# Kernel optimization log

Measured on AMD Instinct MI355X. Metric: run time of the kernel, lower is better.

## Reference

```python
import jax, jax.numpy as jnp
import numpy as np

B, T, HID = 8, 1024, 2048
H, D = 16, 128          # num_attention_heads, head_dim (num_kv_heads = 1)
Q_RANK, KV_RANK = 128, 64
EPS = 1e-6
MIN_VAL = -1e9          # fp32 branch of create_causal_padding_mask


def _rmsnorm(x, w, eps=EPS):
    return x * jax.lax.rsqrt(jnp.mean(x * x, axis=-1, keepdims=True) + eps) * w


def _rope(x, cos, sin):
    x1, x2 = jnp.split(x, 2, axis=-1)
    return jnp.concatenate([x1 * cos - x2 * sin, x2 * cos + x1 * sin], axis=-1)


def setup_inputs() -> dict:
    key = jax.random.key(0)
    ks = jax.random.split(key, 12)
    s = lambda fan_in: 1.0 / np.sqrt(fan_in)
    return {
        'hidden_states': jax.random.normal(ks[0], (B, T, HID), jnp.float32),
        'cos_g': jax.random.uniform(ks[1], (1, T, 1, D // 2), jnp.float32, -1.0, 1.0),
        'sin_g': jax.random.uniform(ks[2], (1, T, 1, D // 2), jnp.float32, -1.0, 1.0),
        'cos_l': jax.random.uniform(ks[3], (1, T, 1, D // 2), jnp.float32, -1.0, 1.0),
        'sin_l': jax.random.uniform(ks[4], (1, T, 1, D // 2), jnp.float32, -1.0, 1.0),
        'Wq_a': jax.random.normal(ks[5], (HID, Q_RANK), jnp.float32) * s(HID),
        'bq_a': jnp.zeros((Q_RANK,), jnp.float32),
        'Wq_b': jax.random.normal(ks[6], (Q_RANK, H * D), jnp.float32) * s(Q_RANK),
        'bq_b': jnp.zeros((H * D,), jnp.float32),
        'Wkv_a': jax.random.normal(ks[7], (HID, KV_RANK), jnp.float32) * s(HID),
        'bkv_a': jnp.zeros((KV_RANK,), jnp.float32),
        'Wkv_b': jax.random.normal(ks[8], (KV_RANK, 2 * D), jnp.float32) * s(KV_RANK),
        'bkv_b': jnp.zeros((2 * D,), jnp.float32),
        'q_norm_w': jnp.ones((D,), jnp.float32),
        'kv_norm_w': jnp.ones((KV_RANK,), jnp.float32),
        'Wo': jax.random.normal(ks[9], (H * D, HID), jnp.float32) * s(H * D),
        'nope_logit': jnp.array([-2.0], jnp.float32),
        'gl_logit': jnp.array([np.log(0.01 / 0.99)], jnp.float32),
        'attention_mask': jnp.ones((B, T), jnp.int32),
    }


def reference(hidden_states, cos_g, sin_g, cos_l, sin_l,
              Wq_a, bq_a, Wq_b, bq_b, Wkv_a, bkv_a, Wkv_b, bkv_b,
              q_norm_w, kv_norm_w, Wo, nope_logit, gl_logit, attention_mask):
    h = hidden_states
    # learned global/local RoPE blend
    a = jax.nn.sigmoid(gl_logit).reshape(1, 1, 1, 1)
    cos = cos_g * a + cos_l * (1.0 - a)
    sin = sin_g * a + sin_l * (1.0 - a)

    # LoRA q path: q_b(RMSNorm(q_a(h)))
    q = _rmsnorm(h @ Wq_a + bq_a, q_norm_w) @ Wq_b + bq_b      # [B,T,H*D]
    q = q.reshape(B, T, H, D)
    q_pe = _rope(q, cos, sin)

    # LoRA kv path: kv_b(RMSNorm(kv_a(h)))  (single kv head)
    kv = _rmsnorm(h @ Wkv_a + bkv_a, kv_norm_w) @ Wkv_b + bkv_b  # [B,T,2*D]
    k, v = jnp.split(kv, 2, axis=-1)                            # [B,T,D] each
    k_pe = _rope(k.reshape(B, T, 1, D), cos, sin)[:, :, 0, :]   # [B,T,D]

    # nope/rope alpha mix
    na = jax.nn.sigmoid(nope_logit).reshape(1, 1, 1, 1)
    q_f = na * q + (1.0 - na) * q_pe                            # [B,T,H,D]
    k_f = na[..., 0] * k + (1.0 - na[..., 0]) * k_pe            # [B,T,D]

    # causal + padding additive mask
    causal = jnp.triu(jnp.ones((T, T), bool), k=1)              # [T,T]
    pad = (attention_mask == 0)[:, None, None, :]               # [B,1,1,T]
    add_mask = jnp.where(causal[None, None] | pad, MIN_VAL, 0.0).astype(h.dtype)

    scale = D ** -0.5
    scores = jnp.einsum('bthd,bsd->bhts', q_f, k_f) * scale + add_mask
    attn = jax.nn.softmax(scores, axis=-1)                      # [B,H,T,T]
    out = jnp.einsum('bhts,bsd->bthd', attn, v)                 # [B,T,H,D]
    return out.reshape(B, T, H * D) @ Wo
```

## Files before the change

kernel.cpp:

```cpp
#include <hip/hip_runtime.h>
#include <hip/hip_bf16.h>

typedef __attribute__((ext_vector_type(8))) short bf16x8;
typedef __attribute__((ext_vector_type(4))) float f32x4;
typedef __attribute__((ext_vector_type(4))) unsigned short us4;

#define DEV __device__ __forceinline__

constexpr int Bc = 8, Tc = 1024, HIDc = 2048, Hc = 16, Dc = 128;
constexpr int ROWSc = Bc * Tc;

DEV unsigned short f2bfb(float x) {
  union { float f; unsigned u; } v; v.f = x;
  unsigned r = v.u + 0x7fffu + ((v.u >> 16) & 1u);
  return (unsigned short)(r >> 16);
}
DEV float bfb2f(unsigned short b) {
  union { unsigned u; float f; } v; v.u = ((unsigned)b) << 16; return v.f;
}
DEV float fexp2(float x) { return __builtin_amdgcn_exp2f(x); }
DEV unsigned pkbf(float lo, float hi) {
  union { float f; unsigned u; } a, b; a.f = lo; b.f = hi;
  return ((b.u + 0x8000u) & 0xffff0000u) | ((a.u + 0x8000u) >> 16);
}

DEV void gload16(const void* g, void* l) {
  __builtin_amdgcn_global_load_lds(
      (const __attribute__((address_space(1))) unsigned int*)g,
      (__attribute__((address_space(3))) unsigned int*)l, 16, 0, 0);
}


__global__ void k_blend(const float* __restrict__ cg, const float* __restrict__ sg,
                        const float* __restrict__ cl, const float* __restrict__ sl,
                        const float* __restrict__ gl,
                        float* __restrict__ cosb, float* __restrict__ sinb) {
  int u = blockIdx.x * 256 + threadIdx.x;
  if (u >= Tc * 64) return;
  float a = 1.0f / (1.0f + __expf(-gl[0]));
  cosb[u] = cg[u] * a + cl[u] * (1.0f - a);
  sinb[u] = sg[u] * a + sl[u] * (1.0f - a);
}

__global__ void k_zero(unsigned short* __restrict__ p, int n) {
  int i = blockIdx.x * 256 + threadIdx.x;
  if (i < n) p[i] = 0;
}

__global__ __launch_bounds__(256) void k_transpose(const float* __restrict__ in,
                                                   unsigned short* __restrict__ out,
                                                   int R, int C) {
  __shared__ float tile[32][33];
  int tx = threadIdx.x & 31, ty = threadIdx.x >> 5;
  int r0 = blockIdx.y * 32, c0 = blockIdx.x * 32;
#pragma unroll
  for (int i = 0; i < 4; i++)
    tile[ty + i * 8][tx] = in[(size_t)(r0 + ty + i * 8) * C + c0 + tx];
  __syncthreads();
#pragma unroll
  for (int i = 0; i < 4; i++) {
    int rr = ty + i * 8;
    out[(size_t)(c0 + rr) * R + r0 + tx] = f2bfb(tile[tx][rr]);
  }
}


__global__ __launch_bounds__(256) void k_gemm1(const float* __restrict__ A,
                                               const unsigned short* __restrict__ Bt,
                                               float* __restrict__ C0,
                                               float* __restrict__ C1) {
  constexpr int K = 2048, N = 256, KH = 1024, NT = KH / 32;
  __shared__ __align__(16) unsigned short Als[2][64 * 32];
  __shared__ __align__(16) unsigned short Bls[2][128 * 32];
  int lin = blockIdx.x;
  int wg = (lin & 7) * 64 + (lin >> 3);
  int ksl = wg & 1;
  int nti = (wg >> 1) & 1;
  int mti = wg >> 2;
  int m0 = mti * 64, n0 = nti * 128, k0 = ksl * KH;
  float* C = ksl ? C1 : C0;
  int tid = threadIdx.x, lane = tid & 63, wc = tid >> 6;
  int ar = tid >> 2, akc = (tid & 3) * 8;
  const float* Ag = A + (size_t)(m0 + ar) * K + k0 + akc;
  const unsigned short* Bg0 = Bt + (size_t)(n0 + ar) * K + k0 + akc;
  const unsigned short* Bg1 = Bt + (size_t)(n0 + 64 + ar) * K + k0 + akc;
  f32x4 acc[4][2];
  f32x4 zz = {0.f, 0.f, 0.f, 0.f};
#pragma unroll
  for (int m = 0; m < 4; m++)
#pragma unroll
    for (int n = 0; n < 2; n++) acc[m][n] = zz;
  int fr = lane & 15, fk = (lane >> 4) * 8;

  float4 a0 = *(const float4*)(Ag);
  float4 a1 = *(const float4*)(Ag + 4);
  gload16(Bg0, &Bls[0][tid * 8]);
  gload16(Bg1, &Bls[0][2048 + tid * 8]);
  {
    us4 c0v = { f2bfb(a0.x), f2bfb(a0.y), f2bfb(a0.z), f2bfb(a0.w) };
    us4 c1v = { f2bfb(a1.x), f2bfb(a1.y), f2bfb(a1.z), f2bfb(a1.w) };
    *(us4*)&Als[0][ar * 32 + akc] = c0v;
    *(us4*)&Als[0][ar * 32 + akc + 4] = c1v;
  }
  a0 = *(const float4*)(Ag + 32);
  a1 = *(const float4*)(Ag + 36);
  __syncthreads();

  for (int t = 0; t < NT; t++) {
    int cur = t & 1, nxt = cur ^ 1;
    if (t + 1 < NT) {
      gload16(Bg0 + (t + 1) * 32, &Bls[nxt][tid * 8]);
      gload16(Bg1 + (t + 1) * 32, &Bls[nxt][2048 + tid * 8]);
    }
    bf16x8 af[4], bfv[2];
#pragma unroll
    for (int i = 0; i < 4; i++)
      af[i] = *(const bf16x8*)&Als[cur][(i * 16 + fr) * 32 + fk];
#pragma unroll
    for (int i = 0; i < 2; i++)
      bfv[i] = *(const bf16x8*)&Bls[cur][(wc * 32 + i * 16 + fr) * 32 + fk];
    __builtin_amdgcn_s_setprio(1);
#pragma unroll
    for (int m = 0; m < 4; m++)
#pragma unroll
      for (int n = 0; n < 2; n++)
        acc[m][n] = __builtin_amdgcn_mfma_f32_16x16x32_bf16(af[m], bfv[n], acc[m][n], 0, 0, 0);
    __builtin_amdgcn_s_setprio(0);
    if (t + 1 < NT) {
      us4 d0 = { f2bfb(a0.x), f2bfb(a0.y), f2bfb(a0.z), f2bfb(a0.w) };
      us4 d1 = { f2bfb(a1.x), f2bfb(a1.y), f2bfb(a1.z), f2bfb(a1.w) };
      *(us4*)&Als[nxt][ar * 32 + akc] = d0;
      *(us4*)&Als[nxt][ar * 32 + akc + 4] = d1;
    }
    if (t + 2 < NT) {
      a0 = *(const float4*)(Ag + (t + 2) * 32);
      a1 = *(const float4*)(Ag + (t + 2) * 32 + 4);
    }
    __syncthreads();
  }
  int gg = lane >> 4;
#pragma unroll
  for (int m = 0; m < 4; m++)
#pragma unroll
    for (int n = 0; n < 2; n++)
#pragma unroll
      for (int r = 0; r < 4; r++) {
        size_t row = (size_t)m0 + m * 16 + gg * 4 + r;
        size_t col = (size_t)n0 + wc * 32 + n * 16 + fr;
        C[row * N + col] = acc[m][n][r];
      }
}


__global__ __launch_bounds__(512, 2) void k_gemm3(const unsigned short* __restrict__ A,
                                                  const unsigned short* __restrict__ Bt,
                                                  float* __restrict__ C) {
  constexpr int K = 2048, N = 2048, NT = K / 64;
  __shared__ __align__(16) unsigned short Als[2][2][8192];
  __shared__ __align__(16) unsigned short Bls[2][2][8192];
  int lin = blockIdx.x;
  int wg = (lin & 7) * 32 + (lin >> 3);
  int m0 = (wg >> 3) * 256, n0 = (wg & 7) * 256;
  int tid = threadIdx.x, lane = tid & 63, wave = tid >> 6;
  int wm = wave >> 2, wn = wave & 3;
  int g = lane >> 4, c = lane & 15;

  int rb = tid >> 2;
  int sch = (tid & 3) ^ ((tid >> 3) & 3);
  const unsigned short* Ag = A + (size_t)(m0 + rb) * K + sch * 8;
  const unsigned short* Bg = Bt + (size_t)(n0 + rb) * K + sch * 8;
  const int gsw = (g ^ ((c >> 1) & 3)) * 8;

  f32x4 acc[8][4];
  f32x4 zz = {0.f, 0.f, 0.f, 0.f};
#pragma unroll
  for (int mi = 0; mi < 8; mi++)
#pragma unroll
    for (int ni = 0; ni < 4; ni++) acc[mi][ni] = zz;

#pragma unroll
  for (int sl = 0; sl < 2; sl++) {
    gload16(Ag + sl * 32, &Als[0][sl][tid * 8]);
    gload16(Ag + (size_t)128 * K + sl * 32, &Als[0][sl][4096 + tid * 8]);
    gload16(Bg + sl * 32, &Bls[0][sl][tid * 8]);
    gload16(Bg + (size_t)128 * K + sl * 32, &Bls[0][sl][4096 + tid * 8]);
  }

  for (int t = 0; t < NT; ++t) {
    int buf = t & 1, nb = buf ^ 1;
    bool nl = (t + 1 < NT);
    int nkt = (t + 1) * 64;
#pragma unroll
    for (int sl = 0; sl < 2; sl++) {
      if (sl == 0 || nl) {
        asm volatile("s_waitcnt vmcnt(4)" ::: "memory");
      } else {
        asm volatile("s_waitcnt vmcnt(0)" ::: "memory");
      }
      __builtin_amdgcn_sched_barrier(0);
      __builtin_amdgcn_s_barrier();
      __builtin_amdgcn_sched_barrier(0);
      const unsigned short* As_ = &Als[buf][sl][0];
      const unsigned short* Bs_ = &Bls[buf][sl][0];
      bf16x8 af[8], bfv[4];
#pragma unroll
      for (int mi = 0; mi < 8; mi++)
        af[mi] = *(const bf16x8*)&As_[(wm * 128 + mi * 16 + c) * 32 + gsw];
#pragma unroll
      for (int ni = 0; ni < 4; ni++)
        bfv[ni] = *(const bf16x8*)&Bs_[(wn * 64 + ni * 16 + c) * 32 + gsw];
      if (nl) {
        gload16(Ag + nkt + sl * 32, &Als[nb][sl][tid * 8]);
        gload16(Ag + (size_t)128 * K + nkt + sl * 32, &Als[nb][sl][4096 + tid * 8]);
      }
      __builtin_amdgcn_s_setprio(1);
#pragma unroll
      for (int mi = 0; mi < 8; mi++) {
        acc[mi][0] = __builtin_amdgcn_mfma_f32_16x16x32_bf16(af[mi], bfv[0], acc[mi][0], 0, 0, 0);
        acc[mi][1] = __builtin_amdgcn_mfma_f32_16x16x32_bf16(af[mi], bfv[1], acc[mi][1], 0, 0, 0);
      }
      __builtin_amdgcn_s_setprio(0);
      if (nl) {
        gload16(Bg + nkt + sl * 32, &Bls[nb][sl][tid * 8]);
        gload16(Bg + (size_t)128 * K + nkt + sl * 32, &Bls[nb][sl][4096 + tid * 8]);
      }
      __builtin_amdgcn_s_setprio(1);
#pragma unroll
      for (int mi = 0; mi < 8; mi++) {
        acc[mi][2] = __builtin_amdgcn_mfma_f32_16x16x32_bf16(af[mi], bfv[2], acc[mi][2], 0, 0, 0);
        acc[mi][3] = __builtin_amdgcn_mfma_f32_16x16x32_bf16(af[mi], bfv[3], acc[mi][3], 0, 0, 0);
      }
      __builtin_amdgcn_s_setprio(0);
    }
  }

#pragma unroll
  for (int mi = 0; mi < 8; mi++)
#pragma unroll
    for (int ni = 0; ni < 4; ni++)
#pragma unroll
      for (int r = 0; r < 4; r++) {
        size_t row = (size_t)m0 + wm * 128 + mi * 16 + g * 4 + r;
        size_t col = (size_t)n0 + wn * 64 + ni * 16 + c;
        C[row * N + col] = acc[mi][ni][r];
      }
}


__global__ __launch_bounds__(256) void k_gemm2q(const unsigned short* __restrict__ A,
                                                const unsigned short* __restrict__ Bt,
                                                const float* __restrict__ bqb,
                                                const float* __restrict__ cosb,
                                                const float* __restrict__ sinb,
                                                const float* __restrict__ nl,
                                                unsigned short* __restrict__ Qf) {
  constexpr int K = 128, N = 2048, NT = 4;
  __shared__ __align__(16) unsigned short As[2][4096];
  __shared__ __align__(16) unsigned short Bs[2][4096];
  __shared__ __align__(16) unsigned short Qt[128 * 128];
  int lin = blockIdx.x;
  int wg = (lin & 7) * 128 + (lin >> 3);
  int m0 = (wg >> 4) * 128, n0 = (wg & 15) * 128;
  int h = n0 >> 7;
  int b = m0 >> 10, t0 = m0 & 1023;
  int tid = threadIdx.x;
  int lane = tid & 63;
  int wave = tid >> 6;
  int wr = wave >> 1, wc = wave & 1;
  int srow = tid >> 2;
  int skc = (tid & 3) * 8;
  const unsigned short* Ag0 = A + (size_t)(m0 + srow) * K + skc;
  const unsigned short* Ag1 = A + (size_t)(m0 + 64 + srow) * K + skc;
  const unsigned short* Bg0 = Bt + (size_t)(n0 + srow) * K + skc;
  const unsigned short* Bg1 = Bt + (size_t)(n0 + 64 + srow) * K + skc;
  f32x4 acc[4][4];
  f32x4 zz = {0.f, 0.f, 0.f, 0.f};
#pragma unroll
  for (int m = 0; m < 4; m++)
#pragma unroll
    for (int n = 0; n < 4; n++) acc[m][n] = zz;
  int fr = lane & 15, fk = (lane >> 4) * 8;

  gload16(Ag0, &As[0][tid * 8]);
  gload16(Ag1, &As[0][2048 + tid * 8]);
  gload16(Bg0, &Bs[0][tid * 8]);
  gload16(Bg1, &Bs[0][2048 + tid * 8]);
  __syncthreads();

  for (int t = 0; t < NT; t++) {
    int cur = t & 1, nxt = cur ^ 1;
    if (t + 1 < NT) {
      int kt = (t + 1) * 32;
      gload16(Ag0 + kt, &As[nxt][tid * 8]);
      gload16(Ag1 + kt, &As[nxt][2048 + tid * 8]);
      gload16(Bg0 + kt, &Bs[nxt][tid * 8]);
      gload16(Bg1 + kt, &Bs[nxt][2048 + tid * 8]);
    }
    bf16x8 af[4], bfv[4];
#pragma unroll
    for (int i = 0; i < 4; i++)
      af[i] = *(const bf16x8*)&As[cur][(wr * 64 + i * 16 + fr) * 32 + fk];
#pragma unroll
    for (int i = 0; i < 4; i++)
      bfv[i] = *(const bf16x8*)&Bs[cur][(wc * 64 + i * 16 + fr) * 32 + fk];
    __builtin_amdgcn_s_setprio(1);
#pragma unroll
    for (int m = 0; m < 4; m++)
#pragma unroll
      for (int n = 0; n < 4; n++)
        acc[m][n] = __builtin_amdgcn_mfma_f32_16x16x32_bf16(af[m], bfv[n], acc[m][n], 0, 0, 0);
    __builtin_amdgcn_s_setprio(0);
    __syncthreads();
  }
  int gg = lane >> 4;
#pragma unroll
  for (int n = 0; n < 4; n++) {
    int col = wc * 64 + n * 16 + fr;
    float bias = bqb[h * 128 + col];
    int ch = col >> 3, wi = col & 7;
#pragma unroll
    for (int m = 0; m < 4; m++)
#pragma unroll
      for (int r = 0; r < 4; r++) {
        int lrow = wr * 64 + m * 16 + gg * 4 + r;
        Qt[lrow * 128 + ((ch ^ (lrow & 7)) << 3) + wi] = f2bfb(acc[m][n][r] + bias);
      }
  }
  __syncthreads();
  const float SCLQ = 0.08838834764831845f * 1.4426950408889634f;
  float na = 1.0f / (1.0f + __expf(-nl[0]));
  float nb = 1.0f - na;
#pragma unroll
  for (int it = 0; it < 4; it++) {
    int task = it * 256 + tid;
    int lrow = task >> 3, cp = task & 7;
    int t = t0 + lrow;
    bf16x8 v1 = *(const bf16x8*)&Qt[lrow * 128 + ((cp ^ (lrow & 7)) << 3)];
    bf16x8 v2 = *(const bf16x8*)&Qt[lrow * 128 + (((cp + 8) ^ (lrow & 7)) << 3)];
    float4 cA = *(const float4*)(cosb + t * 64 + cp * 8);
    float4 cB = *(const float4*)(cosb + t * 64 + cp * 8 + 4);
    float4 sA = *(const float4*)(sinb + t * 64 + cp * 8);
    float4 sB = *(const float4*)(sinb + t * 64 + cp * 8 + 4);
    float cv[8] = {cA.x, cA.y, cA.z, cA.w, cB.x, cB.y, cB.z, cB.w};
    float sv[8] = {sA.x, sA.y, sA.z, sA.w, sB.x, sB.y, sB.z, sB.w};
    float f1[8], f2[8];
#pragma unroll
    for (int j = 0; j < 8; j++) {
      float q1 = bfb2f((unsigned short)v1[j]);
      float q2 = bfb2f((unsigned short)v2[j]);
      float p1 = q1 * cv[j] - q2 * sv[j];
      float p2 = q2 * cv[j] + q1 * sv[j];
      f1[j] = (na * q1 + nb * p1) * SCLQ;
      f2[j] = (na * q2 + nb * p2) * SCLQ;
    }
    unsigned short* ob = Qf + ((size_t)(b * Hc + h) * Tc + t) * Dc + cp * 8;
    us4 o0 = {f2bfb(f1[0]), f2bfb(f1[1]), f2bfb(f1[2]), f2bfb(f1[3])};
    us4 o1 = {f2bfb(f1[4]), f2bfb(f1[5]), f2bfb(f1[6]), f2bfb(f1[7])};
    us4 o2 = {f2bfb(f2[0]), f2bfb(f2[1]), f2bfb(f2[2]), f2bfb(f2[3])};
    us4 o3 = {f2bfb(f2[4]), f2bfb(f2[5]), f2bfb(f2[6]), f2bfb(f2[7])};
    *(us4*)(ob) = o0;
    *(us4*)(ob + 4) = o1;
    *(us4*)(ob + 64) = o2;
    *(us4*)(ob + 68) = o3;
  }
}


__global__ __launch_bounds__(256) void k_gemm2kv(const unsigned short* __restrict__ A,
                                                 const unsigned short* __restrict__ Bt,
                                                 const float* __restrict__ bkvb,
                                                 const float* __restrict__ cosb,
                                                 const float* __restrict__ sinb,
                                                 const float* __restrict__ nl,
                                                 unsigned short* __restrict__ Kf,
                                                 unsigned short* __restrict__ Vt) {
  __shared__ __align__(16) unsigned short As2[64 * 64];
  __shared__ __align__(16) unsigned short Bs2[256 * 64];
  __shared__ __align__(16) unsigned short KVt[64 * 256];
  int m0 = blockIdx.x * 64;
  int b = m0 >> 10, t0 = m0 & 1023;
  int tid = threadIdx.x, lane = tid & 63, wc = tid >> 6;
  int fr = lane & 15, gg = lane >> 4;
#pragma unroll
  for (int p = 0; p < 2; p++) {
    int slot = p * 256 + tid;
    int row = slot >> 3, chpos = slot & 7;
    gload16(A + (size_t)(m0 + row) * 64 + ((chpos ^ (row & 7)) << 3),
            &As2[slot * 8]);
  }
#pragma unroll
  for (int p = 0; p < 8; p++) {
    int slot = p * 256 + tid;
    int row = slot >> 3, chpos = slot & 7;
    gload16(Bt + (size_t)row * 64 + ((chpos ^ (row & 7)) << 3),
            &Bs2[slot * 8]);
  }
  __syncthreads();
  f32x4 acc[4][4];
  f32x4 zz = {0.f, 0.f, 0.f, 0.f};
#pragma unroll
  for (int m = 0; m < 4; m++)
#pragma unroll
    for (int n = 0; n < 4; n++) acc[m][n] = zz;
#pragma unroll
  for (int ks = 0; ks < 2; ks++) {
    bf16x8 af[4], bfv[4];
#pragma unroll
    for (int m = 0; m < 4; m++) {
      int row = m * 16 + fr;
      af[m] = *(const bf16x8*)&As2[row * 64 + (((ks * 4 + gg) ^ (row & 7)) << 3)];
    }
#pragma unroll
    for (int n = 0; n < 4; n++) {
      int row = wc * 64 + n * 16 + fr;
      bfv[n] = *(const bf16x8*)&Bs2[row * 64 + (((ks * 4 + gg) ^ (row & 7)) << 3)];
    }
#pragma unroll
    for (int m = 0; m < 4; m++)
#pragma unroll
      for (int n = 0; n < 4; n++)
        acc[m][n] = __builtin_amdgcn_mfma_f32_16x16x32_bf16(af[m], bfv[n], acc[m][n], 0, 0, 0);
  }
#pragma unroll
  for (int n = 0; n < 4; n++) {
    int col = wc * 64 + n * 16 + fr;
    float bias = bkvb[col];
#pragma unroll
    for (int m = 0; m < 4; m++)
#pragma unroll
      for (int r = 0; r < 4; r++) {
        int lrow = m * 16 + gg * 4 + r;
        KVt[lrow * 256 + col] = f2bfb(acc[m][n][r] + bias);
      }
  }
  __syncthreads();
  float na = 1.0f / (1.0f + __expf(-nl[0]));
  float nb = 1.0f - na;
#pragma unroll
  for (int it = 0; it < 16; it++) {
    int idx = it * 256 + tid;
    int row = idx >> 6, d = idx & 63;
    int t = t0 + row;
    float k1 = bfb2f(KVt[row * 256 + d]);
    float k2 = bfb2f(KVt[row * 256 + 64 + d]);
    float cv = cosb[t * 64 + d], sv = sinb[t * 64 + d];
    float p1 = k1 * cv - k2 * sv;
    float p2 = k2 * cv + k1 * sv;
    unsigned short* kb = Kf + ((size_t)(b * Tc) + t) * Dc;
    kb[d] = f2bfb(na * k1 + nb * p1);
    kb[64 + d] = f2bfb(na * k2 + nb * p2);
  }
  {
    int d = tid & 127, half = tid >> 7;
    unsigned short* vb = Vt + ((size_t)(b * Dc) + d) * Tc + t0 + half * 32;
#pragma unroll
    for (int j = 0; j < 8; j++) {
      int tl = half * 32 + j * 4;
      us4 o = { KVt[(tl + 0) * 256 + 128 + d], KVt[(tl + 1) * 256 + 128 + d],
                KVt[(tl + 2) * 256 + 128 + d], KVt[(tl + 3) * 256 + 128 + d] };
      *(us4*)(vb + j * 4) = o;
    }
  }
}


__global__ __launch_bounds__(256) void k_norm(const float* __restrict__ A1,
                                              const float* __restrict__ A1b,
                                              const float* __restrict__ bqa,
                                              const float* __restrict__ bkva,
                                              const float* __restrict__ qw,
                                              const float* __restrict__ kvw,
                                              unsigned short* __restrict__ Qn,
                                              unsigned short* __restrict__ Kvn) {
  int wave = threadIdx.x >> 6, lane = threadIdx.x & 63;
  int row = blockIdx.x * 4 + wave;
  const float* a = A1 + (size_t)row * 256;
  const float* a2 = A1b + (size_t)row * 256;
  float x0 = a[lane] + a2[lane] + bqa[lane];
  float x1 = a[64 + lane] + a2[64 + lane] + bqa[64 + lane];
  float ss = x0 * x0 + x1 * x1;
#pragma unroll
  for (int off = 1; off < 64; off <<= 1) ss += __shfl_xor(ss, off);
  float sc = rsqrtf(ss * (1.0f / 128.0f) + 1e-6f);
  Qn[(size_t)row * 128 + lane] = f2bfb(x0 * sc * qw[lane]);
  Qn[(size_t)row * 128 + 64 + lane] = f2bfb(x1 * sc * qw[64 + lane]);
  float y = a[128 + lane] + a2[128 + lane] + bkva[lane];
  float s2 = y * y;
#pragma unroll
  for (int off = 1; off < 64; off <<= 1) s2 += __shfl_xor(s2, off);
  float sc2 = rsqrtf(s2 * (1.0f / 64.0f) + 1e-6f);
  Kvn[(size_t)row * 64 + lane] = f2bfb(y * sc2 * kvw[lane]);
}


__global__ __launch_bounds__(512, 1) void k_attn(const unsigned short* __restrict__ Qf,
                                                 const unsigned short* __restrict__ Kf,
                                                 const unsigned short* __restrict__ Vt,
                                                 const int* __restrict__ amask,
                                                 unsigned short* __restrict__ O) {
  __shared__ __align__(16) unsigned short Ks[2][64 * 128];
  __shared__ __align__(16) unsigned short Vs[2][128 * 64];
  __shared__ __align__(16) unsigned short Plds[8][32 * 64];
  __shared__ int s_anyzero;

  int bid = blockIdx.x;
  int b = bid & 7;
  int pr = (bid >> 3) & 1;
  int h = bid >> 4;
  int tid = threadIdx.x;
  int wave = tid >> 6, lane = tid & 63;
  int g = lane >> 4, c = lane & 15;

  const unsigned short* Kp = Kf + (size_t)b * Tc * Dc;
  const unsigned short* Vp = Vt + (size_t)b * Dc * Tc;
  const int* mp = amask + b * Tc;
  char* PwB = (char*)&Plds[wave][0];
  f32x4 zz = {0.f, 0.f, 0.f, 0.f};

  if (tid == 0) s_anyzero = 0;
  __syncthreads();
  if (mp[tid] == 0 || mp[tid + 512] == 0) s_anyzero = 1;
  __syncthreads();
  bool anyz = (s_anyzero != 0);

  int kr_ = tid >> 3, kc_ = tid & 7;
  int vr_ = tid >> 2, vc_ = tid & 3;
  int kidx0 = kr_ * 128 + ((kc_ ^ (kr_ & 7)) << 3);
  int kidx1 = kr_ * 128 + (((kc_ + 8) ^ (kr_ & 7)) << 3);
  int vidx0 = vr_ * 64 + ((vc_ ^ (vr_ & 7)) << 3);
  int vidx1 = vr_ * 64 + (((vc_ + 4) ^ (vr_ & 7)) << 3);

  int c7s = (c & 7) << 4;
  int g4 = g * 4;

  for (int pass = 0; pass < 2; pass++) {
    int sp = (pass == 0) ? pr : 3 - pr;
    int qw0 = sp * 256 + wave * 32;
    int nt = (sp + 1) * 4;
    const unsigned short* Qp = Qf + ((size_t)(b * Hc + h) * Tc + qw0) * Dc;
    bf16x8 qfr[2][4];
#pragma unroll
    for (int m = 0; m < 2; m++)
#pragma unroll
      for (int ks = 0; ks < 4; ks++)
        qfr[m][ks] = *(const bf16x8*)(Qp + (size_t)(m * 16 + c) * Dc + ks * 32 + g * 8);

    f32x4 Oacc[2][8];
#pragma unroll
    for (int m = 0; m < 2; m++)
#pragma unroll
      for (int i = 0; i < 8; i++) Oacc[m][i] = zz;
    float m_r[2] = {-1e30f, -1e30f};
    float l_r[2] = {0.f, 0.f};

    bf16x8 krg[2], vrg[2];
    krg[0] = *(const bf16x8*)(Kp + (size_t)kr_ * Dc + kc_ * 8);
    krg[1] = *(const bf16x8*)(Kp + (size_t)kr_ * Dc + kc_ * 8 + 64);
    vrg[0] = *(const bf16x8*)(Vp + (size_t)vr_ * Tc + vc_ * 8);
    vrg[1] = *(const bf16x8*)(Vp + (size_t)vr_ * Tc + vc_ * 8 + 32);
    __syncthreads();
    *(bf16x8*)&Ks[0][kidx0] = krg[0];
    *(bf16x8*)&Ks[0][kidx1] = krg[1];
    *(bf16x8*)&Vs[0][vidx0] = vrg[0];
    *(bf16x8*)&Vs[0][vidx1] = vrg[1];
    __syncthreads();

    for (int st = 0; st < nt; st++) {
      int cur = st & 1;
      int s0 = st << 6;
      if (st + 1 < nt) {
        int s1 = s0 + 64;
        krg[0] = *(const bf16x8*)(Kp + (size_t)(s1 + kr_) * Dc + kc_ * 8);
        krg[1] = *(const bf16x8*)(Kp + (size_t)(s1 + kr_) * Dc + kc_ * 8 + 64);
        vrg[0] = *(const bf16x8*)(Vp + (size_t)vr_ * Tc + s1 + vc_ * 8);
        vrg[1] = *(const bf16x8*)(Vp + (size_t)vr_ * Tc + s1 + vc_ * 8 + 32);
      }

      if (s0 <= qw0 + 31) {
        const unsigned short* Kc = &Ks[cur][0];
        const unsigned short* Vc = &Vs[cur][0];

        f32x4 S[2][4];
#pragma unroll
        for (int m = 0; m < 2; m++)
#pragma unroll
          for (int j = 0; j < 4; j++) S[m][j] = zz;
        __builtin_amdgcn_s_setprio(1);
#pragma unroll
        for (int ks = 0; ks < 4; ks++)
#pragma unroll
          for (int j = 0; j < 4; j++) {
            bf16x8 kfr = *(const bf16x8*)&Kc[(j * 16 + c) * 128 + (((ks * 4 + g) ^ (c & 7)) << 3)];
            S[0][j] = __builtin_amdgcn_mfma_f32_16x16x32_bf16(kfr, qfr[0][ks], S[0][j], 0, 0, 0);
            S[1][j] = __builtin_amdgcn_mfma_f32_16x16x32_bf16(kfr, qfr[1][ks], S[1][j], 0, 0, 0);
          }
        __builtin_amdgcn_s_setprio(0);

        if (anyz) {
#pragma unroll
          for (int j = 0; j < 4; j++)
#pragma unroll
            for (int r = 0; r < 4; r++) {
              float madd = (mp[s0 + j * 16 + g4 + r] == 0) ? -2e9f : 0.0f;
              S[0][j][r] += madd;
              S[1][j][r] += madd;
            }
        }
        if (s0 + 63 > qw0) {
#pragma unroll
          for (int j = 0; j < 4; j++) {
            int kk = s0 + j * 16 + g4;
#pragma unroll
            for (int r = 0; r < 4; r++) {
#pragma unroll
              for (int m = 0; m < 2; m++)
                if (kk + r > qw0 + m * 16 + c) S[m][j][r] = -1e30f;
            }
          }
        }

        float tmax[2];
#pragma unroll
        for (int m = 0; m < 2; m++) {
          float t0 = fmaxf(fmaxf(S[m][0][0], S[m][0][1]), fmaxf(S[m][0][2], S[m][0][3]));
          float t1 = fmaxf(fmaxf(S[m][1][0], S[m][1][1]), fmaxf(S[m][1][2], S[m][1][3]));
          float t2 = fmaxf(fmaxf(S[m][2][0], S[m][2][1]), fmaxf(S[m][2][2], S[m][2][3]));
          float t3 = fmaxf(fmaxf(S[m][3][0], S[m][3][1]), fmaxf(S[m][3][2], S[m][3][3]));
          float t = fmaxf(fmaxf(t0, t1), fmaxf(t2, t3));
          t = fmaxf(t, __shfl_xor(t, 16));
          t = fmaxf(t, __shfl_xor(t, 32));
          tmax[m] = t;
        }
        bool upd = (tmax[0] > m_r[0] + 11.0f) || (tmax[1] > m_r[1] + 11.0f);
        if (__any(upd)) {
#pragma unroll
          for (int m = 0; m < 2; m++) {
            float mn = fmaxf(m_r[m], tmax[m]);
            float al = fexp2(m_r[m] - mn);
            m_r[m] = mn;
            l_r[m] *= al;
#pragma unroll
            for (int r = 0; r < 4; r++) {
              float alr = __shfl(al, (lane & 48) | (g4 + r));
#pragma unroll
              for (int j2 = 0; j2 < 8; j2++) Oacc[m][j2][r] *= alr;
            }
          }
        }

#pragma unroll
        for (int m = 0; m < 2; m++) {
          int rowb = (m * 16 + c) * 128;
#pragma unroll
          for (int j = 0; j < 4; j++) {
            float e0 = fexp2(S[m][j][0] - m_r[m]);
            float e1 = fexp2(S[m][j][1] - m_r[m]);
            float e2 = fexp2(S[m][j][2] - m_r[m]);
            float e3 = fexp2(S[m][j][3] - m_r[m]);
            l_r[m] += (e0 + e1) + (e2 + e3);
            uint2 w;
            w.x = pkbf(e0, e1);
            w.y = pkbf(e2, e3);
            int inrow = (j * 32 + g * 8) ^ c7s;
            *(uint2*)(PwB + rowb + inrow) = w;
          }
        }

        asm volatile("s_waitcnt lgkmcnt(0)" ::: "memory");
        bf16x8 pa[2][2];
#pragma unroll
        for (int m = 0; m < 2; m++)
#pragma unroll
          for (int sk = 0; sk < 2; sk++)
            pa[m][sk] = *(const bf16x8*)(PwB + (m * 16 + c) * 128 + (((sk * 64 + g * 16)) ^ c7s));
        __builtin_amdgcn_s_setprio(1);
#pragma unroll
        for (int sk = 0; sk < 2; sk++)
#pragma unroll
          for (int j2 = 0; j2 < 8; j2++) {
            int row = j2 * 16 + c;
            bf16x8 vfr = *(const bf16x8*)&Vc[row * 64 + (((sk * 4 + g) ^ (row & 7)) << 3)];
            Oacc[0][j2] = __builtin_amdgcn_mfma_f32_16x16x32_bf16(pa[0][sk], vfr, Oacc[0][j2], 0, 0, 0);
            Oacc[1][j2] = __builtin_amdgcn_mfma_f32_16x16x32_bf16(pa[1][sk], vfr, Oacc[1][j2], 0, 0, 0);
          }
        __builtin_amdgcn_s_setprio(0);
      }

      if (st + 1 < nt) {
        int nxt = cur ^ 1;
        *(bf16x8*)&Ks[nxt][kidx0] = krg[0];
        *(bf16x8*)&Ks[nxt][kidx1] = krg[1];
        *(bf16x8*)&Vs[nxt][vidx0] = vrg[0];
        *(bf16x8*)&Vs[nxt][vidx1] = vrg[1];
      }
      __syncthreads();
    }

#pragma unroll
    for (int m = 0; m < 2; m++) {
      float lt = l_r[m];
      lt += __shfl_xor(lt, 16);
      lt += __shfl_xor(lt, 32);
      float inv = 1.0f / lt;
#pragma unroll
      for (int r = 0; r < 4; r++) {
        float invr = __shfl(inv, (lane & 48) | (g4 + r));
        int qr = qw0 + m * 16 + g4 + r;
        unsigned short* ob = O + ((size_t)(b * Tc) + qr) * HIDc + h * Dc;
#pragma unroll
        for (int j2 = 0; j2 < 8; j2++) ob[j2 * 16 + c] = f2bfb(Oacc[m][j2][r] * invr);
      }
    }
  }
}


extern "C" void kernel_launch(void* const* d_in, const int* in_sizes, int n_in,
                              void* d_out, int out_size, void* d_ws, size_t ws_size,
                              hipStream_t stream) {
  const float* h = (const float*)d_in[0];
  const float* cg = (const float*)d_in[1];
  const float* sg = (const float*)d_in[2];
  const float* cl = (const float*)d_in[3];
  const float* sl = (const float*)d_in[4];
  const float* Wq_a = (const float*)d_in[5];
  const float* bq_a = (const float*)d_in[6];
  const float* Wq_b = (const float*)d_in[7];
  const float* bq_b = (const float*)d_in[8];
  const float* Wkv_a = (const float*)d_in[9];
  const float* bkv_a = (const float*)d_in[10];
  const float* Wkv_b = (const float*)d_in[11];
  const float* bkv_b = (const float*)d_in[12];
  const float* qw = (const float*)d_in[13];
  const float* kvw = (const float*)d_in[14];
  const float* Wo = (const float*)d_in[15];
  const float* nl = (const float*)d_in[16];
  const float* gl = (const float*)d_in[17];
  const int* am = (const int*)d_in[18];
  float* out = (float*)d_out;
  char* ws = (char*)d_ws;

  const size_t o_hB = 0;
  const size_t o_A1b = 33554432;
  const size_t o_Qf = 67108864;
  const size_t o_A1 = 100663296;
  const size_t o_Qn = 109051904;
  const size_t o_Kvn = 111149056;
  const size_t o_Kf = 116391936;
  const size_t o_Vt = 118489088;
  const size_t o_W1t = 120586240;
  const size_t o_Wqbt = 121634816;
  const size_t o_Wkbt = 122159104;
  const size_t o_Wot = 122191872;
  const size_t o_cos = 130580480;
  const size_t o_sin = 130842624;

  unsigned short* Obuf = (unsigned short*)(ws + o_hB);
  float* A1b = (float*)(ws + o_A1b);
  unsigned short* Qf = (unsigned short*)(ws + o_Qf);
  float* A1 = (float*)(ws + o_A1);
  unsigned short* Qn = (unsigned short*)(ws + o_Qn);
  unsigned short* Kvn = (unsigned short*)(ws + o_Kvn);
  unsigned short* Kf = (unsigned short*)(ws + o_Kf);
  unsigned short* Vt = (unsigned short*)(ws + o_Vt);
  unsigned short* W1t = (unsigned short*)(ws + o_W1t);
  unsigned short* Wqbt = (unsigned short*)(ws + o_Wqbt);
  unsigned short* Wkbt = (unsigned short*)(ws + o_Wkbt);
  unsigned short* Wot = (unsigned short*)(ws + o_Wot);
  float* cosb = (float*)(ws + o_cos);
  float* sinb = (float*)(ws + o_sin);

  (void)in_sizes; (void)n_in; (void)out_size; (void)ws_size;

  k_blend<<<256, 256, 0, stream>>>(cg, sg, cl, sl, gl, cosb, sinb);
  k_zero<<<512, 256, 0, stream>>>(W1t + (size_t)192 * 2048, 64 * 2048);
  k_transpose<<<dim3(4, 64), 256, 0, stream>>>(Wq_a, W1t, 2048, 128);
  k_transpose<<<dim3(2, 64), 256, 0, stream>>>(Wkv_a, W1t + (size_t)128 * 2048, 2048, 64);
  k_transpose<<<dim3(64, 4), 256, 0, stream>>>(Wq_b, Wqbt, 128, 2048);
  k_transpose<<<dim3(8, 2), 256, 0, stream>>>(Wkv_b, Wkbt, 64, 256);
  k_transpose<<<dim3(64, 64), 256, 0, stream>>>(Wo, Wot, 2048, 2048);

  k_gemm1<<<512, 256, 0, stream>>>(h, W1t, A1, A1b);
  k_norm<<<2048, 256, 0, stream>>>(A1, A1b, bq_a, bkv_a, qw, kvw, Qn, Kvn);
  k_gemm2q<<<1024, 256, 0, stream>>>(Qn, Wqbt, bq_b, cosb, sinb, nl, Qf);
  k_gemm2kv<<<128, 256, 0, stream>>>(Kvn, Wkbt, bkv_b, cosb, sinb, nl, Kf, Vt);
  k_attn<<<256, 512, 0, stream>>>(Qf, Kf, Vt, am, Obuf);
  k_gemm3<<<256, 512, 0, stream>>>(Obuf, Wot, out);
}
```

Measured before the change: 206.2 us.

## Deepen output GEMM pipeline to four-stage ring of 32-wide K slices

The Wo projection GEMM moves from a double buffer of 64-wide K tiles (two 32-wide sub-slices each) to a four-slot ring of 32-wide K slices. Global loads run three slices ahead, with vmcnt waits adjusted for the last iterations. The B fragments for the second half are now read from LDS after the first MFMA batch, which shortens register live ranges. LDS footprint stays the same, but there is one barrier per 32-wide slice, so barrier count per K is unchanged and prefetch depth grows.

```diff
diff --git a/kernel.cpp b/kernel.cpp
--- a/kernel.cpp
+++ b/kernel.cpp
@@ -155,9 +155,9 @@
 __global__ __launch_bounds__(512, 2) void k_gemm3(const unsigned short* __restrict__ A,
                                                   const unsigned short* __restrict__ Bt,
                                                   float* __restrict__ C) {
-  constexpr int K = 2048, N = 2048, NT = K / 64;
-  __shared__ __align__(16) unsigned short Als[2][2][8192];
-  __shared__ __align__(16) unsigned short Bls[2][2][8192];
+  constexpr int K = 2048, N = 2048, NT = K / 32;
+  __shared__ __align__(16) unsigned short Als[4][8192];
+  __shared__ __align__(16) unsigned short Bls[4][8192];
   int lin = blockIdx.x;
   int wg = (lin & 7) * 32 + (lin >> 3);
   int m0 = (wg >> 3) * 256, n0 = (wg & 7) * 256;
@@ -179,59 +179,60 @@
     for (int ni = 0; ni < 4; ni++) acc[mi][ni] = zz;
 
 #pragma unroll
-  for (int sl = 0; sl < 2; sl++) {
-    gload16(Ag + sl * 32, &Als[0][sl][tid * 8]);
-    gload16(Ag + (size_t)128 * K + sl * 32, &Als[0][sl][4096 + tid * 8]);
-    gload16(Bg + sl * 32, &Bls[0][sl][tid * 8]);
-    gload16(Bg + (size_t)128 * K + sl * 32, &Bls[0][sl][4096 + tid * 8]);
+  for (int t = 0; t < 3; t++) {
+    gload16(Ag + t * 32, &Als[t][tid * 8]);
+    gload16(Ag + (size_t)128 * K + t * 32, &Als[t][4096 + tid * 8]);
+    gload16(Bg + t * 32, &Bls[t][tid * 8]);
+    gload16(Bg + (size_t)128 * K + t * 32, &Bls[t][4096 + tid * 8]);
   }
 
   for (int t = 0; t < NT; ++t) {
-    int buf = t & 1, nb = buf ^ 1;
-    bool nl = (t + 1 < NT);
-    int nkt = (t + 1) * 64;
-#pragma unroll
-    for (int sl = 0; sl < 2; sl++) {
-      if (sl == 0 || nl) {
-        asm volatile("s_waitcnt vmcnt(4)" ::: "memory");
-      } else {
-        asm volatile("s_waitcnt vmcnt(0)" ::: "memory");
-      }
-      __builtin_amdgcn_sched_barrier(0);
-      __builtin_amdgcn_s_barrier();
-      __builtin_amdgcn_sched_barrier(0);
-      const unsigned short* As_ = &Als[buf][sl][0];
-      const unsigned short* Bs_ = &Bls[buf][sl][0];
-      bf16x8 af[8], bfv[4];
-#pragma unroll
-      for (int mi = 0; mi < 8; mi++)
-        af[mi] = *(const bf16x8*)&As_[(wm * 128 + mi * 16 + c) * 32 + gsw];
-#pragma unroll
-      for (int ni = 0; ni < 4; ni++)
-        bfv[ni] = *(const bf16x8*)&Bs_[(wn * 64 + ni * 16 + c) * 32 + gsw];
-      if (nl) {
-        gload16(Ag + nkt + sl * 32, &Als[nb][sl][tid * 8]);
-        gload16(Ag + (size_t)128 * K + nkt + sl * 32, &Als[nb][sl][4096 + tid * 8]);
-      }
-      __builtin_amdgcn_s_setprio(1);
-#pragma unroll
-      for (int mi = 0; mi < 8; mi++) {
-        acc[mi][0] = __builtin_amdgcn_mfma_f32_16x16x32_bf16(af[mi], bfv[0], acc[mi][0], 0, 0, 0);
-        acc[mi][1] = __builtin_amdgcn_mfma_f32_16x16x32_bf16(af[mi], bfv[1], acc[mi][1], 0, 0, 0);
-      }
-      __builtin_amdgcn_s_setprio(0);
-      if (nl) {
-        gload16(Bg + nkt + sl * 32, &Bls[nb][sl][tid * 8]);
-        gload16(Bg + (size_t)128 * K + nkt + sl * 32, &Bls[nb][sl][4096 + tid * 8]);
-      }
-      __builtin_amdgcn_s_setprio(1);
-#pragma unroll
-      for (int mi = 0; mi < 8; mi++) {
-        acc[mi][2] = __builtin_amdgcn_mfma_f32_16x16x32_bf16(af[mi], bfv[2], acc[mi][2], 0, 0, 0);
-        acc[mi][3] = __builtin_amdgcn_mfma_f32_16x16x32_bf16(af[mi], bfv[3], acc[mi][3], 0, 0, 0);
-      }
-      __builtin_amdgcn_s_setprio(0);
-    }
+    int buf = t & 3;
+    if (t < NT - 2) {
+      asm volatile("s_waitcnt vmcnt(8)" ::: "memory");
+    } else if (t == NT - 2) {
+      asm volatile("s_waitcnt vmcnt(4)" ::: "memory");
+    } else {
+      asm volatile("s_waitcnt vmcnt(0)" ::: "memory");
+    }
+    __builtin_amdgcn_sched_barrier(0);
+    __builtin_amdgcn_s_barrier();
+    __builtin_amdgcn_sched_barrier(0);
+
+    const unsigned short* As_ = &Als[buf][0];
+    const unsigned short* Bs_ = &Bls[buf][0];
+    bf16x8 af[8], bf01[2], bf23[2];
+#pragma unroll
+    for (int mi = 0; mi < 8; mi++)
+      af[mi] = *(const bf16x8*)&As_[(wm * 128 + mi * 16 + c) * 32 + gsw];
+    bf01[0] = *(const bf16x8*)&Bs_[(wn * 64 + c) * 32 + gsw];
+    bf01[1] = *(const bf16x8*)&Bs_[(wn * 64 + 16 + c) * 32 + gsw];
+    if (t + 3 < NT) {
+      int nkt = (t + 3) * 32, nb = (t + 3) & 3;
+      gload16(Ag + nkt, &Als[nb][tid * 8]);
+      gload16(Ag + (size_t)128 * K + nkt, &Als[nb][4096 + tid * 8]);
+    }
+    __builtin_amdgcn_s_setprio(1);
+#pragma unroll
+    for (int mi = 0; mi < 8; mi++) {
+      acc[mi][0] = __builtin_amdgcn_mfma_f32_16x16x32_bf16(af[mi], bf01[0], acc[mi][0], 0, 0, 0);
+      acc[mi][1] = __builtin_amdgcn_mfma_f32_16x16x32_bf16(af[mi], bf01[1], acc[mi][1], 0, 0, 0);
+    }
+    __builtin_amdgcn_s_setprio(0);
+    bf23[0] = *(const bf16x8*)&Bs_[(wn * 64 + 32 + c) * 32 + gsw];
+    bf23[1] = *(const bf16x8*)&Bs_[(wn * 64 + 48 + c) * 32 + gsw];
+    if (t + 3 < NT) {
+      int nkt = (t + 3) * 32, nb = (t + 3) & 3;
+      gload16(Bg + nkt, &Bls[nb][tid * 8]);
+      gload16(Bg + (size_t)128 * K + nkt, &Bls[nb][4096 + tid * 8]);
+    }
+    __builtin_amdgcn_s_setprio(1);
+#pragma unroll
+    for (int mi = 0; mi < 8; mi++) {
+      acc[mi][2] = __builtin_amdgcn_mfma_f32_16x16x32_bf16(af[mi], bf23[0], acc[mi][2], 0, 0, 0);
+      acc[mi][3] = __builtin_amdgcn_mfma_f32_16x16x32_bf16(af[mi], bf23[1], acc[mi][3], 0, 0, 0);
+    }
+    __builtin_amdgcn_s_setprio(0);
   }
 
 #pragma unroll
```

Result: no change. 205.6 us (-0.3%).
